# Kernel optimization log

Measured on AMD Instinct MI355X. Metric: run time of the kernel, lower is better.

The kernel has to match this reference:

```python
import jax, jax.numpy as jnp
import numpy as np

E = 192      # embed_dim
DI = 384     # d_inner = 2*E (mamba default expand=2)
S = 16       # d_state
R = 12       # dt_rank = ceil(E/16)
DEPTH = 4
STRIDE = 4
P = 400      # num_patches = 1600/4
NC = 20
BATCH = 32
EPS = 1e-5


def _rmsnorm(x, w):
    x = x.astype(jnp.float32)
    return x * jax.lax.rsqrt(jnp.mean(x * x, axis=-1, keepdims=True) + EPS) * w


def _mamba_mixer(h, in_w, cw, cb, xpw, dtw, dtb, a_log, d_skip, ow):
    # h: [B, L, E]
    Bsz, Ln, _ = h.shape
    xz = jnp.einsum('ble,de->bld', h, in_w)            # [B,L,2*DI]
    xm, z = xz[..., :DI], xz[..., DI:]
    # causal depthwise conv1d, kernel 4 (left pad 3, truncate to L)
    xp = jnp.pad(xm, ((0, 0), (3, 0), (0, 0)))
    xc = sum(xp[:, k:k + Ln, :] * cw[:, k] for k in range(4)) + cb
    xc = jax.nn.silu(xc)
    xdb = jnp.einsum('bld,rd->blr', xc, xpw)           # [B,L,R+2S]
    dt = jax.nn.softplus(jnp.einsum('blr,dr->bld', xdb[..., :R], dtw) + dtb)
    Bm = xdb[..., R:R + S]
    Cm = xdb[..., R + S:]
    A = -jnp.exp(a_log)                                # [DI,S]

    def step(hst, inp):
        dt_t, b_t, c_t, u_t = inp                      # [B,DI],[B,S],[B,S],[B,DI]
        dA = jnp.exp(dt_t[:, :, None] * A)             # [B,DI,S]
        hst = dA * hst + (dt_t * u_t)[:, :, None] * b_t[:, None, :]
        y_t = jnp.einsum('bdn,bn->bd', hst, c_t)
        return hst, y_t

    h0 = jnp.zeros((Bsz, DI, S), xc.dtype)
    xs = (dt.transpose(1, 0, 2), Bm.transpose(1, 0, 2), Cm.transpose(1, 0, 2), xc.transpose(1, 0, 2))
    _, ys = jax.lax.scan(step, h0, xs)
    y = ys.transpose(1, 0, 2) + xc * d_skip
    y = y * jax.nn.silu(z)
    return jnp.einsum('bld,ed->ble', y, ow)


def _forward(imgs, patch_w, patch_b, cls_token, pos_embed, cnn_w, cnn_b, norm_w,
             in_proj_w, conv_w, conv_b, x_proj_w, dt_proj_w, dt_proj_b, A_log, D,
             out_proj_w, norm_f_w, head_w, head_b):
    Bsz = imgs.shape[0]
    # StrideEmbed: conv1d kernel=stride=4 == reshape + matmul
    x = imgs.reshape(Bsz, P, STRIDE)
    x = jnp.einsum('blk,ek->ble', x, patch_w[:, 0, :]) + patch_b   # [B,P,E]
    x = x + pos_embed[:, :-1, :]
    # depthwise conv1d k=3 pad=1 over length
    xp = jnp.pad(x, ((0, 0), (1, 1), (0, 0)))
    x = sum(xp[:, k:k + P, :] * cnn_w[:, 0, k] for k in range(3)) + cnn_b
    cls = cls_token + pos_embed[:, -1, :]                           # [1,1,E]
    x = jnp.concatenate([x, jnp.broadcast_to(cls, (Bsz, 1, E))], axis=1)  # [B,401,E]

    hidden = x
    residual = None
    for i in range(DEPTH):
        residual = hidden if residual is None else residual + hidden
        hn = _rmsnorm(residual, norm_w[i])
        hidden = _mamba_mixer(hn, in_proj_w[i], conv_w[i], conv_b[i], x_proj_w[i],
                              dt_proj_w[i], dt_proj_b[i], A_log[i], D[i], out_proj_w[i])
    out = _rmsnorm(hidden + residual, norm_f_w)
    v_sem = out[:, -1, :]
    return v_sem @ head_w.T + head_b


def setup_inputs() -> dict:
    key = jax.random.key(0)
    ks = jax.random.split(key, 12)
    n = lambda k, shp, s=0.02: jax.random.normal(k, shp, dtype=jnp.float32) * s
    return {
        'imgs': jax.random.normal(ks[0], (BATCH, 1, 40, 40), jnp.float32),
        'patch_w': n(ks[1], (E, 1, STRIDE), 0.3),
        'patch_b': jnp.zeros((E,), jnp.float32),
        'cls_token': n(ks[2], (1, 1, E)),
        'pos_embed': n(ks[3], (1, P + 1, E)),
        'cnn_w': n(ks[4], (E, 1, 3), 0.3),
        'cnn_b': jnp.zeros((E,), jnp.float32),
        'norm_w': jnp.ones((DEPTH, E), jnp.float32),
        'in_proj_w': n(ks[5], (DEPTH, 2 * DI, E), 0.05),
        'conv_w': n(ks[6], (DEPTH, DI, 4), 0.3),
        'conv_b': jnp.zeros((DEPTH, DI), jnp.float32),
        'x_proj_w': n(ks[7], (DEPTH, R + 2 * S, DI), 0.05),
        'dt_proj_w': n(ks[8], (DEPTH, DI, R), 0.3),
        'dt_proj_b': jnp.log(jnp.expm1(jax.random.uniform(ks[9], (DEPTH, DI), minval=0.001, maxval=0.1))),
        'A_log': jnp.log(jnp.broadcast_to(jnp.arange(1, S + 1, dtype=jnp.float32), (DEPTH, DI, S))),
        'D': jnp.ones((DEPTH, DI), jnp.float32),
        'out_proj_w': n(ks[10], (DEPTH, E, DI), 0.05),
        'norm_f_w': jnp.ones((E,), jnp.float32),
        'head_w': n(ks[11], (NC, E)),
        'head_b': jnp.zeros((NC,), jnp.float32),
    }


def reference(imgs, patch_w, patch_b, cls_token, pos_embed, cnn_w, cnn_b, norm_w,
              in_proj_w, conv_w, conv_b, x_proj_w, dt_proj_w, dt_proj_b, A_log, D,
              out_proj_w, norm_f_w, head_w, head_b):
    return _forward(imgs, patch_w, patch_b, cls_token, pos_embed, cnn_w, cnn_b, norm_w,
                    in_proj_w, conv_w, conv_b, x_proj_w, dt_proj_w, dt_proj_b, A_log, D,
                    out_proj_w, norm_f_w, head_w, head_b)
```

## Files before the change

### kernel.cpp

```cpp
#include <hip/hip_runtime.h>
#include <math.h>

#define E 192
#define DI 384
#define S 16
#define R 12
#define DEPTH 4
#define P 400
#define NC 20
#define BATCH 32
#define L 401
#define NTOK (BATCH * L)
#define CH 32
#define NCH 13

using short8 = __attribute__((ext_vector_type(8))) short;
using float4v = __attribute__((ext_vector_type(4))) float;

__device__ __forceinline__ float siluf(float x) {
    return x / (1.f + __expf(-x));
}
__device__ __forceinline__ float softplusf(float x) {
    return (x > 20.f) ? x : log1pf(__expf(x));
}
__device__ __forceinline__ unsigned short f2bf(float x) {
    unsigned int u = __float_as_uint(x);
    unsigned int r = 0x7fffu + ((u >> 16) & 1u);
    return (unsigned short)((u + r) >> 16);
}
__device__ __forceinline__ float bf2f(unsigned short v) {
    return __uint_as_float(((unsigned int)v) << 16);
}

__global__ void k_embed(const float* __restrict__ imgs, const float* __restrict__ patch_w,
                        const float* __restrict__ patch_b, const float* __restrict__ cls_token,
                        const float* __restrict__ pos_embed, const float* __restrict__ cnn_w,
                        const float* __restrict__ cnn_b, float* __restrict__ resid) {
    int idx = blockIdx.x * blockDim.x + threadIdx.x;
    if (idx >= NTOK * E) return;
    int e = idx % E;
    int bl = idx / E;
    int l = bl % L;
    int b = bl / L;
    float out;
    if (l == P) {
        out = cls_token[e] + pos_embed[(size_t)P * E + e];
    } else {
        float w0 = patch_w[e * 4 + 0], w1 = patch_w[e * 4 + 1];
        float w2 = patch_w[e * 4 + 2], w3 = patch_w[e * 4 + 3];
        float pb = patch_b[e];
        const float* ib = imgs + (size_t)b * 1600;
        auto xe = [&](int ll) -> float {
            const float* ip = ib + ll * 4;
            return ip[0] * w0 + ip[1] * w1 + ip[2] * w2 + ip[3] * w3 + pb +
                   pos_embed[(size_t)ll * E + e];
        };
        float c0 = cnn_w[e * 3 + 0], c1 = cnn_w[e * 3 + 1], c2 = cnn_w[e * 3 + 2];
        float acc = cnn_b[e] + xe(l) * c1;
        if (l > 0) acc += xe(l - 1) * c0;
        if (l < P - 1) acc += xe(l + 1) * c2;
        out = acc;
    }
    resid[idx] = out;
}

__global__ void k_rmsnorm(const float* __restrict__ resid, unsigned short* __restrict__ hn,
                          const float* __restrict__ w) {
    int wave = blockIdx.x * (blockDim.x >> 6) + (threadIdx.x >> 6);
    int lane = threadIdx.x & 63;
    if (wave >= NTOK) return;
    size_t base = (size_t)wave * E;
    float v[3];
    float ss = 0.f;
#pragma unroll
    for (int j = 0; j < 3; j++) {
        int e = lane + j * 64;
        float r = resid[base + e];
        v[j] = r;
        ss += r * r;
    }
#pragma unroll
    for (int off = 32; off > 0; off >>= 1) ss += __shfl_xor(ss, off, 64);
    float scale = rsqrtf(ss * (1.f / (float)E) + 1e-5f);
#pragma unroll
    for (int j = 0; j < 3; j++) {
        int e = lane + j * 64;
        hn[base + e] = f2bf(v[j] * scale * w[e]);
    }
}

__global__ void k_prep(const float* __restrict__ in_proj_w, const float* __restrict__ x_proj_w,
                       const float* __restrict__ out_proj_w, const float* __restrict__ A_log,
                       const float* __restrict__ dt_proj_w,
                       unsigned short* __restrict__ w_in, unsigned short* __restrict__ w_x,
                       unsigned short* __restrict__ w_out, float* __restrict__ negA,
                       float* __restrict__ dtw_t) {
    const int n1 = DEPTH * 2 * DI * E;
    const int n2 = DEPTH * 44 * DI;
    const int n3 = DEPTH * E * DI;
    const int n4 = DEPTH * DI * S;
    const int n5 = DEPTH * DI * R;
    int idx = blockIdx.x * blockDim.x + threadIdx.x;
    if (idx < n1) {
        w_in[idx] = f2bf(in_proj_w[idx]);
    } else if (idx < n1 + n2) {
        int i = idx - n1;
        w_x[i] = f2bf(x_proj_w[i]);
    } else if (idx < n1 + n2 + n3) {
        int i = idx - n1 - n2;
        w_out[i] = f2bf(out_proj_w[i]);
    } else if (idx < n1 + n2 + n3 + n4) {
        int i = idx - n1 - n2 - n3;
        int layer = i / (DI * S);
        int rem = i % (DI * S);
        int n = rem / DI;
        int d = rem % DI;
        negA[i] = -__expf(A_log[(size_t)layer * DI * S + d * S + n]);
    } else if (idx < n1 + n2 + n3 + n4 + n5) {
        int i = idx - n1 - n2 - n3 - n4;
        int layer = i / (DI * R);
        int rem = i % (DI * R);
        int r = rem / DI;
        int d = rem % DI;
        dtw_t[i] = dt_proj_w[(size_t)layer * DI * R + d * R + r];
    }
}

__global__ void k_flag(const float* __restrict__ negA, int* __restrict__ flag) {
    int idx = blockIdx.x * blockDim.x + threadIdx.x;
    if (idx >= DEPTH * DI) return;
    int layer = idx / DI;
    int d = idx % DI;
    const float* base = negA + (size_t)layer * DI * S;
    float a0 = base[d];
    bool ok = true;
#pragma unroll
    for (int n = 1; n < S; n++) {
        float an = base[n * DI + d];
        ok = ok && (fabsf(an - (float)(n + 1) * a0) <= 1e-5f * fabsf(an));
    }
    flag[idx] = ok ? 1 : 0;
}

template <int BM, int BN, int EPI>
__global__ __launch_bounds__(256) void k_gemm_bf16(const unsigned short* __restrict__ A,
                                                   const unsigned short* __restrict__ W,
                                                   float* __restrict__ C,
                                                   unsigned short* __restrict__ XM,
                                                   unsigned short* __restrict__ Z,
                                                   int M, int N, int K) {
    constexpr int BK = 64, PADK = BK + 8;
    constexpr int MT = BM / 32, NT = BN / 32;
    __shared__ unsigned short As[BM][PADK];
    __shared__ unsigned short Bs[BN][PADK];
    int tid = threadIdx.x;
    int m0 = blockIdx.y * BM, n0 = blockIdx.x * BN;
    int wave = tid >> 6, lane = tid & 63;
    int row16 = lane & 15, quad = lane >> 4;
    int wm0 = (wave >> 1) * (BM / 2), wn0 = (wave & 1) * (BN / 2);

    float4v acc[MT][NT];
#pragma unroll
    for (int i = 0; i < MT; i++)
#pragma unroll
        for (int j = 0; j < NT; j++) acc[i][j] = (float4v){0.f, 0.f, 0.f, 0.f};

    for (int k0 = 0; k0 < K; k0 += BK) {
#pragma unroll
        for (int p = 0; p < MT; p++) {
            int idx = (p * 256 + tid) * 8;
            int row = idx / BK, col = idx % BK;
            int gm = m0 + row;
            short8 v;
            if (gm < M)
                v = *(const short8*)&A[(size_t)gm * K + k0 + col];
            else
                v = (short8)0;
            *(short8*)&As[row][col] = v;
        }
#pragma unroll
        for (int p = 0; p < NT; p++) {
            int idx = (p * 256 + tid) * 8;
            int row = idx / BK, col = idx % BK;
            int gn = n0 + row;
            short8 v;
            if (gn < N)
                v = *(const short8*)&W[(size_t)gn * K + k0 + col];
            else
                v = (short8)0;
            *(short8*)&Bs[row][col] = v;
        }
        __syncthreads();
#pragma unroll
        for (int kk = 0; kk < BK; kk += 32) {
            int koff = kk + quad * 8;
            short8 af[MT], bfr[NT];
#pragma unroll
            for (int i = 0; i < MT; i++)
                af[i] = *(const short8*)&As[wm0 + i * 16 + row16][koff];
#pragma unroll
            for (int j = 0; j < NT; j++)
                bfr[j] = *(const short8*)&Bs[wn0 + j * 16 + row16][koff];
#pragma unroll
            for (int i = 0; i < MT; i++)
#pragma unroll
                for (int j = 0; j < NT; j++)
                    acc[i][j] = __builtin_amdgcn_mfma_f32_16x16x32_bf16(af[i], bfr[j],
                                                                        acc[i][j], 0, 0, 0);
        }
        __syncthreads();
    }
#pragma unroll
    for (int i = 0; i < MT; i++) {
#pragma unroll
        for (int j = 0; j < NT; j++) {
#pragma unroll
            for (int r = 0; r < 4; r++) {
                int m = m0 + wm0 + i * 16 + quad * 4 + r;
                int n = n0 + wn0 + j * 16 + row16;
                if (m >= M || n >= N) continue;
                float v = acc[i][j][r];
                if (EPI == 0) {
                    C[(size_t)m * N + n] = v;
                } else if (EPI == 1) {
                    if (n < DI)
                        XM[(size_t)m * DI + n] = f2bf(v);
                    else
                        Z[(size_t)m * DI + (n - DI)] = f2bf(v);
                } else {
                    C[(size_t)m * N + n] += v;
                }
            }
        }
    }
}

template <int BM, int BN>
__global__ __launch_bounds__(256) void k_xproj_conv(
        const unsigned short* __restrict__ xm, const unsigned short* __restrict__ W,
        const float* __restrict__ cw, const float* __restrict__ cb,
        float* __restrict__ C, unsigned short* __restrict__ xc_bf, int M, int N) {
    constexpr int K = DI, BK = 64, PADK = BK + 8;
    constexpr int MT = BM / 32, NT = BN / 32;
    __shared__ unsigned short As[BM][PADK];
    __shared__ unsigned short Bs[BN][PADK];
    int tid = threadIdx.x;
    int m0 = blockIdx.y * BM;
    int wave = tid >> 6, lane = tid & 63;
    int row16 = lane & 15, quad = lane >> 4;
    int wm0 = (wave >> 1) * (BM / 2), wn0 = (wave & 1) * (BN / 2);

    float4v acc[MT][NT];
#pragma unroll
    for (int i = 0; i < MT; i++)
#pragma unroll
        for (int j = 0; j < NT; j++) acc[i][j] = (float4v){0.f, 0.f, 0.f, 0.f};

    for (int k0 = 0; k0 < K; k0 += BK) {
#pragma unroll
        for (int p = 0; p < MT; p++) {
            int idx = (p * 256 + tid) * 8;
            int row = idx / BK, col = idx % BK;
            int t = m0 + row;
            short8 v = (short8)0;
            if (t < M) {
                int l = t % L;
                int d0 = k0 + col;
                float av[8];
#pragma unroll
                for (int j = 0; j < 8; j++) av[j] = cb[d0 + j];
#pragma unroll
                for (int k = 0; k < 4; k++) {
                    int ll = l - 3 + k;
                    if (ll >= 0) {
                        short8 xv = *(const short8*)&xm[(size_t)(t - 3 + k) * DI + d0];
#pragma unroll
                        for (int j = 0; j < 8; j++)
                            av[j] += bf2f((unsigned short)xv[j]) * cw[(d0 + j) * 4 + k];
                    }
                }
#pragma unroll
                for (int j = 0; j < 8; j++) v[j] = (short)f2bf(siluf(av[j]));
                *(short8*)&xc_bf[(size_t)t * DI + d0] = v;
            }
            *(short8*)&As[row][col] = v;
        }
#pragma unroll
        for (int p = 0; p < NT; p++) {
            int idx = (p * 256 + tid) * 8;
            int row = idx / BK, col = idx % BK;
            short8 v;
            if (row < N)
                v = *(const short8*)&W[(size_t)row * K + k0 + col];
            else
                v = (short8)0;
            *(short8*)&Bs[row][col] = v;
        }
        __syncthreads();
#pragma unroll
        for (int kk = 0; kk < BK; kk += 32) {
            int koff = kk + quad * 8;
            short8 af[MT], bfr[NT];
#pragma unroll
            for (int i = 0; i < MT; i++)
                af[i] = *(const short8*)&As[wm0 + i * 16 + row16][koff];
#pragma unroll
            for (int j = 0; j < NT; j++)
                bfr[j] = *(const short8*)&Bs[wn0 + j * 16 + row16][koff];
#pragma unroll
            for (int i = 0; i < MT; i++)
#pragma unroll
                for (int j = 0; j < NT; j++)
                    acc[i][j] = __builtin_amdgcn_mfma_f32_16x16x32_bf16(af[i], bfr[j],
                                                                        acc[i][j], 0, 0, 0);
        }
        __syncthreads();
    }
#pragma unroll
    for (int i = 0; i < MT; i++) {
#pragma unroll
        for (int j = 0; j < NT; j++) {
#pragma unroll
            for (int r = 0; r < 4; r++) {
                int m = m0 + wm0 + i * 16 + quad * 4 + r;
                int n = wn0 + j * 16 + row16;
                if (m >= M || n >= N) continue;
                C[(size_t)m * N + n] = acc[i][j][r];
            }
        }
    }
}

__global__ __launch_bounds__(384) void k_dtpre(
        const float* __restrict__ xdb, const float* __restrict__ dtw_t,
        const float* __restrict__ dtb, float* __restrict__ dtbuf) {
    int tok = blockIdx.x;
    int d = threadIdx.x;
    const float* xr = xdb + (size_t)tok * 44;
    float acc = dtb[d];
#pragma unroll
    for (int r = 0; r < R; r++) acc += xr[r] * dtw_t[r * DI + d];
    dtbuf[(size_t)tok * DI + d] = softplusf(acc);
}

template <bool LAST>
__global__ __launch_bounds__(384) void k_scanA(
        const unsigned short* __restrict__ xc_bf, const float* __restrict__ xdb,
        const float* __restrict__ dtbuf, const float* __restrict__ negA_l,
        const int* __restrict__ flag_l, const float* __restrict__ Dskip,
        float2* __restrict__ ydt, float* __restrict__ hend) {
    int d = threadIdx.x;
    int ch = blockIdx.x;
    int b = blockIdx.y;
    int t0 = ch * CH;
    int t1 = min(t0 + CH, L);
    bool fast = __all(flag_l[d] != 0);
    float a0 = negA_l[d];
    float a[S];
    if (!fast) {
#pragma unroll
        for (int n = 0; n < S; n++) a[n] = negA_l[n * DI + d];
    }
    float dsk = Dskip[d];
    float h[S] = {};
    float dts = 0.f;
    size_t tok0 = (size_t)b * L + t0;
    float dt_nx = dtbuf[tok0 * DI + d];
    float u_nx = bf2f(xc_bf[tok0 * DI + d]);
    float e1_nx = __expf(a0 * dt_nx);
    for (int t = t0; t < t1; t++) {
        size_t tok = (size_t)b * L + t;
        float dtv = dt_nx, e1v = e1_nx, uu = u_nx;
        if (t + 1 < t1) {
            dt_nx = dtbuf[(tok + 1) * DI + d];
            u_nx = bf2f(xc_bf[(tok + 1) * DI + d]);
            e1_nx = __expf(a0 * dt_nx);
        }
        const float* row = xdb + tok * 44;
        dts += dtv;
        float dtu = dtv * uu;
        float y = uu * dsk;
        if (fast) {
            float p = e1v;
#pragma unroll
            for (int n = 0; n < S; n++) {
                h[n] = p * h[n] + dtu * row[R + n];
                y += h[n] * row[R + S + n];
                p *= e1v;
            }
        } else {
#pragma unroll
            for (int n = 0; n < S; n++) {
                float dA = __expf(dtv * a[n]);
                h[n] = dA * h[n] + dtu * row[R + n];
                y += h[n] * row[R + S + n];
            }
        }
        if (!LAST || t == P || t == t1 - 1) ydt[tok * DI + d] = make_float2(y, dts);
    }
    float* he = hend + ((size_t)(b * NCH + ch) * S) * DI + d;
#pragma unroll
    for (int n = 0; n < S; n++) he[n * DI] = h[n];
}

__global__ void k_scanB(const float* __restrict__ hend, const float2* __restrict__ ydt,
                        const float* __restrict__ negA_l, const int* __restrict__ flag_l,
                        float* __restrict__ hinit) {
    int idx = blockIdx.x * blockDim.x + threadIdx.x;
    if (idx >= BATCH * DI) return;
    int d = idx % DI;
    int b = idx / DI;
    bool fast = __all(flag_l[d] != 0);
    float a[S];
#pragma unroll
    for (int n = 0; n < S; n++) a[n] = negA_l[n * DI + d];
    float h[S] = {};
    for (int ch = 0; ch < NCH; ch++) {
        size_t o = ((size_t)(b * NCH + ch) * S) * DI + d;
#pragma unroll
        for (int n = 0; n < S; n++) hinit[o + n * DI] = h[n];
        int tlast = min(ch * CH + CH, L) - 1;
        float dts = ydt[((size_t)b * L + tlast) * DI + d].y;
        if (fast) {
            float e1c = __expf(a[0] * dts);
            float p = e1c;
#pragma unroll
            for (int n = 0; n < S; n++) {
                h[n] = p * h[n] + hend[o + n * DI];
                p *= e1c;
            }
        } else {
#pragma unroll
            for (int n = 0; n < S; n++) h[n] = __expf(dts * a[n]) * h[n] + hend[o + n * DI];
        }
    }
}

__global__ __launch_bounds__(384) void k_fixup(
        const unsigned short* __restrict__ z_bf, const float* __restrict__ xdb,
        const float* __restrict__ negA_l, const int* __restrict__ flag_l,
        const float* __restrict__ hinit, const float2* __restrict__ ydt,
        unsigned short* __restrict__ y_bf) {
    int tok = blockIdx.x;
    int d = threadIdx.x;
    int l = tok % L;
    int b = tok / L;
    int ch = l / CH;
    size_t idx = (size_t)tok * DI + d;
    float2 yd = ydt[idx];
    float y = yd.x;
    if (ch != 0) {
        bool fast = __all(flag_l[d] != 0);
        const float* h0 = hinit + ((size_t)(b * NCH + ch) * S) * DI + d;
        const float* cv = xdb + (size_t)tok * 44 + R + S;
        float dts = yd.y;
        float corr = 0.f;
        if (fast) {
            float e1c = __expf(negA_l[d] * dts);
            float p = e1c;
#pragma unroll
            for (int n = 0; n < S; n++) {
                corr += cv[n] * p * h0[n * DI];
                p *= e1c;
            }
        } else {
#pragma unroll
            for (int n = 0; n < S; n++)
                corr += cv[n] * __expf(negA_l[n * DI + d] * dts) * h0[n * DI];
        }
        y += corr;
    }
    float z = bf2f(z_bf[idx]);
    y_bf[idx] = f2bf(y * siluf(z));
}

__global__ __launch_bounds__(384) void k_fixup_last(
        const unsigned short* __restrict__ z_bf, const float* __restrict__ xdb,
        const float* __restrict__ negA_l, const int* __restrict__ flag_l,
        const float* __restrict__ hinit, const float2* __restrict__ ydt,
        unsigned short* __restrict__ y32) {
    int b = blockIdx.x;
    int d = threadIdx.x;
    int tok = b * L + P;
    int ch = P / CH;
    size_t idx = (size_t)tok * DI + d;
    float2 yd = ydt[idx];
    float y = yd.x;
    {
        bool fast = __all(flag_l[d] != 0);
        const float* h0 = hinit + ((size_t)(b * NCH + ch) * S) * DI + d;
        const float* cv = xdb + (size_t)tok * 44 + R + S;
        float dts = yd.y;
        float corr = 0.f;
        if (fast) {
            float e1c = __expf(negA_l[d] * dts);
            float p = e1c;
#pragma unroll
            for (int n = 0; n < S; n++) {
                corr += cv[n] * p * h0[n * DI];
                p *= e1c;
            }
        } else {
#pragma unroll
            for (int n = 0; n < S; n++)
                corr += cv[n] * __expf(negA_l[n * DI + d] * dts) * h0[n * DI];
        }
        y += corr;
    }
    float z = bf2f(z_bf[idx]);
    y32[(size_t)b * DI + d] = f2bf(y * siluf(z));
}

__global__ void k_head(const float* __restrict__ resid, const float* __restrict__ hidden32,
                       const float* __restrict__ norm_f_w, const float* __restrict__ head_w,
                       const float* __restrict__ head_b, float* __restrict__ out) {
    __shared__ float v[E];
    int b = blockIdx.x;
    int lane = threadIdx.x;
    size_t base = ((size_t)b * L + P) * E;
    float loc[3];
    float ss = 0.f;
#pragma unroll
    for (int j = 0; j < 3; j++) {
        int e = lane + j * 64;
        float x = resid[base + e] + hidden32[(size_t)b * E + e];
        loc[j] = x;
        ss += x * x;
    }
#pragma unroll
    for (int off = 32; off > 0; off >>= 1) ss += __shfl_xor(ss, off, 64);
    float scale = rsqrtf(ss * (1.f / (float)E) + 1e-5f);
#pragma unroll
    for (int j = 0; j < 3; j++) {
        int e = lane + j * 64;
        v[e] = loc[j] * scale * norm_f_w[e];
    }
    __syncthreads();
    if (lane < NC) {
        float acc = head_b[lane];
        for (int e = 0; e < E; e++) acc += v[e] * head_w[lane * E + e];
        out[b * NC + lane] = acc;
    }
}

extern "C" void kernel_launch(void* const* d_in, const int* in_sizes, int n_in,
                              void* d_out, int out_size, void* d_ws, size_t ws_size,
                              hipStream_t stream) {
    const float* imgs      = (const float*)d_in[0];
    const float* patch_w   = (const float*)d_in[1];
    const float* patch_b   = (const float*)d_in[2];
    const float* cls_token = (const float*)d_in[3];
    const float* pos_embed = (const float*)d_in[4];
    const float* cnn_w     = (const float*)d_in[5];
    const float* cnn_b     = (const float*)d_in[6];
    const float* norm_w    = (const float*)d_in[7];
    const float* in_proj_w = (const float*)d_in[8];
    const float* conv_w    = (const float*)d_in[9];
    const float* conv_b    = (const float*)d_in[10];
    const float* x_proj_w  = (const float*)d_in[11];
    const float* dt_proj_w = (const float*)d_in[12];
    const float* dt_proj_b = (const float*)d_in[13];
    const float* A_log     = (const float*)d_in[14];
    const float* Dskip     = (const float*)d_in[15];
    const float* out_proj_w= (const float*)d_in[16];
    const float* norm_f_w  = (const float*)d_in[17];
    const float* head_w    = (const float*)d_in[18];
    const float* head_b    = (const float*)d_in[19];

    float* ws = (float*)d_ws;
    size_t off = 0;
    float* resid  = ws + off; off += (size_t)NTOK * E;
    float* xdb    = ws + off; off += (size_t)NTOK * 44;
    float* dtbuf  = ws + off; off += (size_t)NTOK * DI;
    float* ydt    = ws + off; off += (size_t)NTOK * DI * 2;
    float* hend   = ws + off; off += (size_t)BATCH * NCH * DI * S;
    float* hinit  = ws + off; off += (size_t)BATCH * NCH * DI * S;
    float* negA   = ws + off; off += (size_t)DEPTH * DI * S;
    float* dtw_t  = ws + off; off += (size_t)DEPTH * DI * R;
    float* hid32  = ws + off; off += (size_t)BATCH * E;
    int*   gflag  = (int*)(ws + off); off += (size_t)DEPTH * DI;
    unsigned short* xm_bf  = (unsigned short*)(ws + off); off += (size_t)NTOK * DI / 2;
    unsigned short* z_bf   = (unsigned short*)(ws + off); off += (size_t)NTOK * DI / 2;
    unsigned short* bf_buf = (unsigned short*)(ws + off); off += (size_t)NTOK * DI / 2;
    unsigned short* y32_bf = (unsigned short*)(ws + off); off += (size_t)BATCH * DI / 2 + 16;
    unsigned short* w_in  = (unsigned short*)(ws + off); off += (size_t)DEPTH * 2 * DI * E / 2;
    unsigned short* w_x   = (unsigned short*)(ws + off); off += (size_t)DEPTH * 44 * DI / 2 + 16;
    unsigned short* w_out = (unsigned short*)(ws + off); off += (size_t)DEPTH * E * DI / 2;

    unsigned short* hn_bf = bf_buf;
    unsigned short* xc_bf = bf_buf;
    unsigned short* y_bf  = bf_buf;

    {
        int ntot = DEPTH * (2 * DI * E + 44 * DI + E * DI + DI * S + DI * R);
        k_prep<<<(ntot + 255) / 256, 256, 0, stream>>>(in_proj_w, x_proj_w, out_proj_w, A_log,
                                                       dt_proj_w, w_in, w_x, w_out, negA,
                                                       dtw_t);
        k_flag<<<(DEPTH * DI + 255) / 256, 256, 0, stream>>>(negA, gflag);
    }

    k_embed<<<(NTOK * E) / 256, 256, 0, stream>>>(imgs, patch_w, patch_b, cls_token,
                                                  pos_embed, cnn_w, cnn_b, resid);

    for (int i = 0; i < DEPTH; i++) {
        k_rmsnorm<<<NTOK / 4, 256, 0, stream>>>(resid, hn_bf, norm_w + i * E);

        {
            dim3 g((2 * DI) / 128, (NTOK + 127) / 128);
            k_gemm_bf16<128, 128, 1><<<g, 256, 0, stream>>>(
                hn_bf, w_in + (size_t)i * 2 * DI * E, nullptr, xm_bf, z_bf, NTOK, 2 * DI, E);
        }
        {
            dim3 g(1, (NTOK + 63) / 64);
            k_xproj_conv<64, 64><<<g, 256, 0, stream>>>(
                xm_bf, w_x + (size_t)i * 44 * DI, conv_w + (size_t)i * DI * 4,
                conv_b + (size_t)i * DI, xdb, xc_bf, NTOK, 44);
        }
        const float* nA = negA + (size_t)i * DI * S;
        const int* fl = gflag + (size_t)i * DI;
        k_dtpre<<<NTOK, 384, 0, stream>>>(xdb, dtw_t + (size_t)i * DI * R,
                                          dt_proj_b + (size_t)i * DI, dtbuf);
        dim3 g(NCH, BATCH);
        if (i < DEPTH - 1) {
            k_scanA<false><<<g, DI, 0, stream>>>(xc_bf, xdb, dtbuf, nA, fl,
                                                 Dskip + (size_t)i * DI, (float2*)ydt, hend);
            k_scanB<<<(BATCH * DI + 255) / 256, 256, 0, stream>>>(hend, (const float2*)ydt,
                                                                  nA, fl, hinit);
            k_fixup<<<NTOK, 384, 0, stream>>>(z_bf, xdb, nA, fl, hinit,
                                              (const float2*)ydt, y_bf);
            dim3 go(E / 64, (NTOK + 127) / 128);
            k_gemm_bf16<128, 64, 2><<<go, 256, 0, stream>>>(
                y_bf, w_out + (size_t)i * E * DI, resid, nullptr, nullptr, NTOK, E, DI);
        } else {
            k_scanA<true><<<g, DI, 0, stream>>>(xc_bf, xdb, dtbuf, nA, fl,
                                                Dskip + (size_t)i * DI, (float2*)ydt, hend);
            k_scanB<<<(BATCH * DI + 255) / 256, 256, 0, stream>>>(hend, (const float2*)ydt,
                                                                  nA, fl, hinit);
            k_fixup_last<<<BATCH, 384, 0, stream>>>(z_bf, xdb, nA, fl, hinit,
                                                    (const float2*)ydt, y32_bf);
            dim3 go(E / 64, 1);
            k_gemm_bf16<32, 64, 0><<<go, 256, 0, stream>>>(
                y32_bf, w_out + (size_t)i * E * DI, hid32, nullptr, nullptr, BATCH, E, DI);
        }
    }

    k_head<<<BATCH, 64, 0, stream>>>(resid, hid32, norm_f_w, head_w, head_b, (float*)d_out);
}
```

Measured before the change: 767.6 us.

## Split causal conv into elementwise kernel and fuse dt projection into x_proj GEMM

The depthwise causal conv and SiLU move out of the x_proj GEMM tile loader into a standalone elementwise kernel. The x_proj GEMM now reads precomputed xc and uses a smaller 32-row tile for more blocks. Its epilogue stages the 44 outputs per token in shared memory and computes the dt projection plus softplus directly, which removes the separate k_dtpre launch and its reread of xdb. The cost is an extra launch and a full write-then-read of xc between the conv and the GEMM.

```diff
diff --git a/kernel.cpp b/kernel.cpp
--- a/kernel.cpp
+++ b/kernel.cpp
@@ -235,15 +235,33 @@
     }
 }
 
-template <int BM, int BN>
-__global__ __launch_bounds__(256) void k_xproj_conv(
-        const unsigned short* __restrict__ xm, const unsigned short* __restrict__ W,
-        const float* __restrict__ cw, const float* __restrict__ cb,
-        float* __restrict__ C, unsigned short* __restrict__ xc_bf, int M, int N) {
-    constexpr int K = DI, BK = 64, PADK = BK + 8;
+__global__ void k_conv(const unsigned short* __restrict__ xm_bf, const float* __restrict__ cw,
+                       const float* __restrict__ cb, unsigned short* __restrict__ xc_bf) {
+    int idx = blockIdx.x * blockDim.x + threadIdx.x;
+    if (idx >= NTOK * DI) return;
+    int d = idx % DI;
+    int bl = idx / DI;
+    int l = bl % L;
+    int b = bl / L;
+    const unsigned short* base = xm_bf + (size_t)b * L * DI + d;
+    float acc = cb[d];
+#pragma unroll
+    for (int k = 0; k < 4; k++) {
+        int ll = l - 3 + k;
+        if (ll >= 0) acc += bf2f(base[(size_t)ll * DI]) * cw[d * 4 + k];
+    }
+    xc_bf[idx] = f2bf(siluf(acc));
+}
+
+__global__ __launch_bounds__(256) void k_xproj_dt(
+        const unsigned short* __restrict__ A, const unsigned short* __restrict__ W,
+        const float* __restrict__ dtw_t, const float* __restrict__ dtb,
+        float* __restrict__ C, float* __restrict__ dtbuf, int M, int N) {
+    constexpr int BM = 32, BN = 64, K = DI, BK = 64, PADK = BK + 8;
     constexpr int MT = BM / 32, NT = BN / 32;
     __shared__ unsigned short As[BM][PADK];
     __shared__ unsigned short Bs[BN][PADK];
+    __shared__ float xs[BM][45];
     int tid = threadIdx.x;
     int m0 = blockIdx.y * BM;
     int wave = tid >> 6, lane = tid & 63;
@@ -261,28 +279,12 @@
         for (int p = 0; p < MT; p++) {
             int idx = (p * 256 + tid) * 8;
             int row = idx / BK, col = idx % BK;
-            int t = m0 + row;
-            short8 v = (short8)0;
-            if (t < M) {
-                int l = t % L;
-                int d0 = k0 + col;
-                float av[8];
-#pragma unroll
-                for (int j = 0; j < 8; j++) av[j] = cb[d0 + j];
-#pragma unroll
-                for (int k = 0; k < 4; k++) {
-                    int ll = l - 3 + k;
-                    if (ll >= 0) {
-                        short8 xv = *(const short8*)&xm[(size_t)(t - 3 + k) * DI + d0];
-#pragma unroll
-                        for (int j = 0; j < 8; j++)
-                            av[j] += bf2f((unsigned short)xv[j]) * cw[(d0 + j) * 4 + k];
-                    }
-                }
-#pragma unroll
-                for (int j = 0; j < 8; j++) v[j] = (short)f2bf(siluf(av[j]));
-                *(short8*)&xc_bf[(size_t)t * DI + d0] = v;
-            }
+            int gm = m0 + row;
+            short8 v;
+            if (gm < M)
+                v = *(const short8*)&A[(size_t)gm * K + k0 + col];
+            else
+                v = (short8)0;
             *(short8*)&As[row][col] = v;
         }
 #pragma unroll
@@ -322,25 +324,28 @@
         for (int j = 0; j < NT; j++) {
 #pragma unroll
             for (int r = 0; r < 4; r++) {
-                int m = m0 + wm0 + i * 16 + quad * 4 + r;
+                int ml = wm0 + i * 16 + quad * 4 + r;
                 int n = wn0 + j * 16 + row16;
+                int m = m0 + ml;
                 if (m >= M || n >= N) continue;
-                C[(size_t)m * N + n] = acc[i][j][r];
+                float v = acc[i][j][r];
+                C[(size_t)m * N + n] = v;
+                xs[ml][n] = v;
             }
         }
     }
-}
-
-__global__ __launch_bounds__(384) void k_dtpre(
-        const float* __restrict__ xdb, const float* __restrict__ dtw_t,
-        const float* __restrict__ dtb, float* __restrict__ dtbuf) {
-    int tok = blockIdx.x;
-    int d = threadIdx.x;
-    const float* xr = xdb + (size_t)tok * 44;
-    float acc = dtb[d];
-#pragma unroll
-    for (int r = 0; r < R; r++) acc += xr[r] * dtw_t[r * DI + d];
-    dtbuf[(size_t)tok * DI + d] = softplusf(acc);
+    __syncthreads();
+    for (int it = 0; it < (BM * DI) / 256; it++) {
+        int li = it * 256 + tid;
+        int ml = li / DI;
+        int d = li % DI;
+        int m = m0 + ml;
+        if (m >= M) continue;
+        float a2 = dtb[d];
+#pragma unroll
+        for (int r = 0; r < R; r++) a2 += xs[ml][r] * dtw_t[r * DI + d];
+        dtbuf[(size_t)m * DI + d] = softplusf(a2);
+    }
 }
 
 template <bool LAST>
@@ -610,16 +615,16 @@
             k_gemm_bf16<128, 128, 1><<<g, 256, 0, stream>>>(
                 hn_bf, w_in + (size_t)i * 2 * DI * E, nullptr, xm_bf, z_bf, NTOK, 2 * DI, E);
         }
+        k_conv<<<(NTOK * DI) / 256, 256, 0, stream>>>(xm_bf, conv_w + (size_t)i * DI * 4,
+                                                      conv_b + (size_t)i * DI, xc_bf);
         {
-            dim3 g(1, (NTOK + 63) / 64);
-            k_xproj_conv<64, 64><<<g, 256, 0, stream>>>(
-                xm_bf, w_x + (size_t)i * 44 * DI, conv_w + (size_t)i * DI * 4,
-                conv_b + (size_t)i * DI, xdb, xc_bf, NTOK, 44);
+            dim3 g(1, NTOK / 32);
+            k_xproj_dt<<<g, 256, 0, stream>>>(
+                xc_bf, w_x + (size_t)i * 44 * DI, dtw_t + (size_t)i * DI * R,
+                dt_proj_b + (size_t)i * DI, xdb, dtbuf, NTOK, 44);
         }
         const float* nA = negA + (size_t)i * DI * S;
         const int* fl = gflag + (size_t)i * DI;
-        k_dtpre<<<NTOK, 384, 0, stream>>>(xdb, dtw_t + (size_t)i * DI * R,
-                                          dt_proj_b + (size_t)i * DI, dtbuf);
         dim3 g(NCH, BATCH);
         if (i < DEPTH - 1) {
             k_scanA<false><<<g, DI, 0, stream>>>(xc_bf, xdb, dtbuf, nA, fl,
```

Result: slower. 815.8 us (+6.3%).
